# Kernel optimization log

Measured on AMD Instinct MI355X. Metric: run time of the kernel, lower is better.

The kernel has to match this reference:

```python
import jax, jax.numpy as jnp
import numpy as np

ANCHORS = np.array([[1.4940052559648322, 2.3598481287086823],
                    [4.0113013115312155, 5.760873975661669]], dtype=np.float32)
THRESH = 0.6
OBJ_SCALE = 5.0
NOOBJ_SCALE = 1.0


def setup_inputs() -> dict:
    key = jax.random.key(0)
    k1, k2, k3 = jax.random.split(key, 3)
    nB, nA, nH, nW = 128, 2, 128, 128
    output = jax.random.normal(k1, (nB, nA * 5, nH, nW), dtype=jnp.float32)
    xy = jax.random.uniform(k2, (nB, 2), jnp.float32, 0.1, 0.9)   # box centers, normalized
    wh = jax.random.uniform(k3, (nB, 2), jnp.float32, 0.05, 0.4)  # box sizes, normalized
    target = jnp.concatenate([xy, wh], axis=1)  # [nB, 4] = (x, y, w, h)
    anchors = jnp.asarray(ANCHORS)
    return {"output": output, "target": target, "anchors": anchors}


def reference(output, target, anchors):
    nB, _, nH, nW = output.shape
    nA = anchors.shape[0]
    # [nB, nA, nH, nW, 5]
    out = output.reshape(nB, nA, 5, nH, nW).transpose(0, 1, 3, 4, 2)
    x = jax.nn.sigmoid(out[..., 0])
    y = jax.nn.sigmoid(out[..., 1])
    w = out[..., 2]
    h = out[..., 3]
    conf = jax.nn.sigmoid(out[..., 4])

    # torch code uses .data / Variable() everywhere in target construction -> no grads flow there
    tgt = jax.lax.stop_gradient(target)
    anc = jax.lax.stop_gradient(anchors)
    sg = jax.lax.stop_gradient

    fW = jnp.asarray(nW, dtype=x.dtype)
    fH = jnp.asarray(nH, dtype=x.dtype)
    grid_x = jnp.arange(nW, dtype=x.dtype)[None, None, None, :]
    grid_y = jnp.arange(nH, dtype=x.dtype)[None, None, :, None]
    aw = anc[:, 0][None, :, None, None]
    ah = anc[:, 1][None, :, None, None]

    # detached predicted boxes in grid units (cx, cy, w, h)
    pb_x = sg(x) + grid_x
    pb_y = sg(y) + grid_y
    pb_w = jnp.exp(sg(w)) * aw
    pb_h = jnp.exp(sg(h)) * ah

    gt_x = tgt[:, 0] * fW
    gt_y = tgt[:, 1] * fH
    gt_w = tgt[:, 2] * fW
    gt_h = tgt[:, 3] * fH
    gx4 = gt_x[:, None, None, None]
    gy4 = gt_y[:, None, None, None]
    gw4 = gt_w[:, None, None, None]
    gh4 = gt_h[:, None, None, None]

    # vectorized bbox_iou (x1y1x2y2=False), faithful to the scalar torch loop
    mx = jnp.minimum(pb_x - pb_w * 0.5, gx4 - gw4 * 0.5)
    Mx = jnp.maximum(pb_x + pb_w * 0.5, gx4 + gw4 * 0.5)
    my = jnp.minimum(pb_y - pb_h * 0.5, gy4 - gh4 * 0.5)
    My = jnp.maximum(pb_y + pb_h * 0.5, gy4 + gh4 * 0.5)
    uw = Mx - mx
    uh = My - my
    cw = pb_w + gw4 - uw
    ch = pb_h + gh4 - uh
    carea = cw * ch
    uarea = pb_w * pb_h + gw4 * gh4 - carea
    iou = jnp.where((cw <= 0) | (ch <= 0), jnp.zeros((), x.dtype), carea / uarea)

    noobj_mask = iou <= THRESH  # [nB, nA, nH, nW]

    # best anchor per GT via wh-IoU (bbox_anchor_iou)
    inter = jnp.minimum(gt_w[:, None], anc[None, :, 0]) * jnp.minimum(gt_h[:, None], anc[None, :, 1])
    union = gt_w[:, None] * gt_h[:, None] + 1e-16 + anc[None, :, 0] * anc[None, :, 1] - inter
    best_n = jnp.argmax(inter / union, axis=1)  # [nB]

    gxi = gt_x.astype(jnp.int32)
    gyi = gt_y.astype(jnp.int32)
    b_idx = jnp.arange(nB)
    noobj_mask = noobj_mask.at[b_idx, best_n, gyi, gxi].set(False)

    tx = gt_x - jnp.floor(gt_x)
    ty = gt_y - jnp.floor(gt_y)
    tw = jnp.log(gt_w / anc[best_n, 0] + 1e-16)
    th = jnp.log(gt_h / anc[best_n, 1] + 1e-16)
    scale = 2.0 - tgt[:, 2] * tgt[:, 3]  # [nB]

    x_s = x[b_idx, best_n, gyi, gxi]
    y_s = y[b_idx, best_n, gyi, gxi]
    w_s = w[b_idx, best_n, gyi, gxi]
    h_s = h[b_idx, best_n, gyi, gxi]
    conf_s = conf[b_idx, best_n, gyi, gxi]

    loss_x = jnp.mean((x_s * scale - tx * scale) ** 2)
    loss_y = jnp.mean((y_s * scale - ty * scale) ** 2)
    loss_w = jnp.mean((w_s * scale - tw * scale) ** 2)
    loss_h = jnp.mean((h_s * scale - th * scale) ** 2)

    n_noobj = jnp.sum(noobj_mask).astype(conf.dtype)
    loss_conf = (OBJ_SCALE * jnp.mean((conf_s - 1.0) ** 2)
                 + NOOBJ_SCALE * jnp.sum(jnp.where(noobj_mask, conf * conf, 0.0)) / n_noobj)

    return loss_x + loss_y + loss_w + loss_h + loss_conf
```

## Files before the change

kernel.cpp:

```cpp
#include <hip/hip_runtime.h>

#define NB 128
#define NA 2
#define NH 128
#define NW 128
#define PLANE (NH * NW)
#define RTHRESH 0.6f
#define OBJ_SCALE 5.0f
#define NBLK 1024

__device__ __forceinline__ float sigm(float v) {
    return 1.0f / (1.0f + __expf(-v));
}

__device__ __forceinline__ void batch_const(const float* __restrict__ target,
                                            const float* __restrict__ anchors,
                                            int b,
                                            float& gx, float& gy, float& gw, float& gh,
                                            int& bn, int& gxi, int& gyi) {
    float t0 = target[b * 4 + 0], t1 = target[b * 4 + 1];
    float t2 = target[b * 4 + 2], t3 = target[b * 4 + 3];
    gx = t0 * (float)NW;
    gy = t1 * (float)NH;
    gw = t2 * (float)NW;
    gh = t3 * (float)NH;
    float a0w = anchors[0], a0h = anchors[1];
    float a1w = anchors[2], a1h = anchors[3];
    float i0 = fminf(gw, a0w) * fminf(gh, a0h);
    float u0 = gw * gh + 1e-16f + a0w * a0h - i0;
    float i1 = fminf(gw, a1w) * fminf(gh, a1h);
    float u1 = gw * gh + 1e-16f + a1w * a1h - i1;
    bn  = (i1 / u1 > i0 / u0) ? 1 : 0;
    gxi = (int)gx;
    gyi = (int)gy;
}

__global__ __launch_bounds__(256) void region_main(
        const float* __restrict__ out,
        const float* __restrict__ target,
        const float* __restrict__ anchors,
        float* __restrict__ psum,
        unsigned int* __restrict__ pcnt) {
    int bid = blockIdx.x, tid = threadIdx.x;
    int slab = bid >> 2, q = bid & 3;
    int b = slab >> 1, a = slab & 1;

    float gx, gy, gw, gh; int bn, gxi, gyi;
    batch_const(target, anchors, b, gx, gy, gw, gh, bn, gxi, gyi);
    float aw = anchors[a * 2 + 0];
    float ah = anchors[a * 2 + 1];

    const float* pb = out + (size_t)(b * 10 + a * 5) * PLANE + q * 4096 + tid * 4;

    float4 vx[4], vy[4], vw[4], vh[4], vc[4];
#pragma unroll
    for (int it = 0; it < 4; ++it) {
        const float* p = pb + it * 1024;
        vx[it] = *(const float4*)(p);
        vy[it] = *(const float4*)(p + 1 * PLANE);
        vw[it] = *(const float4*)(p + 2 * PLANE);
        vh[it] = *(const float4*)(p + 3 * PLANE);
        vc[it] = *(const float4*)(p + 4 * PLANE);
    }

    float gxm = gx - gw * 0.5f, gxM = gx + gw * 0.5f;
    float gym = gy - gh * 0.5f, gyM = gy + gh * 0.5f;
    float garea = gw * gh;
    bool a_sel = (a == bn);

    float lsum = 0.0f;
    int   lcnt = 0;

#pragma unroll
    for (int it = 0; it < 4; ++it) {
        const float* fx = (const float*)&vx[it];
        const float* fy = (const float*)&vy[it];
        const float* fw = (const float*)&vw[it];
        const float* fh = (const float*)&vh[it];
        const float* fc = (const float*)&vc[it];
        int pos0 = q * 4096 + it * 1024 + tid * 4;
#pragma unroll
        for (int e = 0; e < 4; ++e) {
            int pos = pos0 + e;
            int j = pos & 127, i = pos >> 7;
            float px = sigm(fx[e]) + (float)j;
            float py = sigm(fy[e]) + (float)i;
            float pw = __expf(fw[e]) * aw;
            float ph = __expf(fh[e]) * ah;
            float cf = sigm(fc[e]);

            float mx = fminf(px - pw * 0.5f, gxm);
            float Mx = fmaxf(px + pw * 0.5f, gxM);
            float my = fminf(py - ph * 0.5f, gym);
            float My = fmaxf(py + ph * 0.5f, gyM);
            float cw = pw + gw - (Mx - mx);
            float ch = ph + gh - (My - my);
            float iou = 0.0f;
            if (cw > 0.0f && ch > 0.0f) {
                float carea = cw * ch;
                iou = carea / (pw * ph + garea - carea);
            }
            bool noobj = (iou <= RTHRESH) && !(a_sel && i == gyi && j == gxi);
            if (noobj) { lsum += cf * cf; lcnt += 1; }
        }
    }

#pragma unroll
    for (int off = 32; off > 0; off >>= 1) {
        lsum += __shfl_down(lsum, off);
        lcnt += __shfl_down(lcnt, off);
    }
    __shared__ float ssum[4];
    __shared__ int   scnt[4];
    int wid = tid >> 6, lane = tid & 63;
    if (lane == 0) { ssum[wid] = lsum; scnt[wid] = lcnt; }
    __syncthreads();
    if (tid == 0) {
        psum[bid] = ssum[0] + ssum[1] + ssum[2] + ssum[3];
        pcnt[bid] = (unsigned int)(scnt[0] + scnt[1] + scnt[2] + scnt[3]);
    }
}

__global__ __launch_bounds__(1024) void region_final(
        const float* __restrict__ out,
        const float* __restrict__ target,
        const float* __restrict__ anchors,
        const float* __restrict__ psum,
        const unsigned int* __restrict__ pcnt,
        float* __restrict__ loss_out) {
    int t = threadIdx.x;
    float s = psum[t];
    unsigned int c = pcnt[t];

    float v = 0.0f;
    if (t < NB) {
        int b = t;
        float gx, gy, gw, gh; int bn, gxi, gyi;
        batch_const(target, anchors, b, gx, gy, gw, gh, bn, gxi, gyi);
        float tx = gx - floorf(gx);
        float ty = gy - floorf(gy);
        float aw = anchors[bn * 2 + 0];
        float ah = anchors[bn * 2 + 1];
        float tw = __logf(gw / aw + 1e-16f);
        float th = __logf(gh / ah + 1e-16f);
        float scale = 2.0f - target[b * 4 + 2] * target[b * 4 + 3];

        size_t base = (size_t)(b * 10 + bn * 5) * PLANE + (size_t)gyi * NW + (size_t)gxi;
        float xs = sigm(out[base]);
        float ys = sigm(out[base + 1 * PLANE]);
        float wr = out[base + 2 * PLANE];
        float hr = out[base + 3 * PLANE];
        float cs = sigm(out[base + 4 * PLANE]);

        float dx = (xs - tx) * scale;
        float dy = (ys - ty) * scale;
        float dw = (wr - tw) * scale;
        float dh = (hr - th) * scale;
        float dc = cs - 1.0f;
        v = dx * dx + dy * dy + dw * dw + dh * dh + OBJ_SCALE * dc * dc;
    }

#pragma unroll
    for (int off = 32; off > 0; off >>= 1) {
        s += __shfl_down(s, off);
        c += __shfl_down(c, off);
        v += __shfl_down(v, off);
    }
    __shared__ float ss[16];
    __shared__ unsigned int sc[16];
    __shared__ float sv[16];
    int wid = t >> 6, lane = t & 63;
    if (lane == 0) { ss[wid] = s; sc[wid] = c; sv[wid] = v; }
    __syncthreads();
    if (t < 16) {
        s = ss[t]; c = sc[t]; v = sv[t];
#pragma unroll
        for (int off = 8; off > 0; off >>= 1) {
            s += __shfl_down(s, off);
            c += __shfl_down(c, off);
            v += __shfl_down(v, off);
        }
        if (t == 0)
            loss_out[0] = v * (1.0f / (float)NB) + s / (float)c;
    }
}

extern "C" void kernel_launch(void* const* d_in, const int* in_sizes, int n_in,
                              void* d_out, int out_size, void* d_ws, size_t ws_size,
                              hipStream_t stream) {
    const float* output  = (const float*)d_in[0];
    const float* target  = (const float*)d_in[1];
    const float* anchors = (const float*)d_in[2];
    float* loss = (float*)d_out;

    float* psum = (float*)d_ws;
    unsigned int* pcnt = (unsigned int*)((char*)d_ws + NBLK * sizeof(float));

    region_main<<<NBLK, 256, 0, stream>>>(output, target, anchors, psum, pcnt);
    region_final<<<1, 1024, 0, stream>>>(output, target, anchors, psum, pcnt, loss);
}
```

Measured before the change: 124.9 us.

## Replace IoU division with multiply compare, use fast reciprocal sigmoid, prefetch per step

The IoU threshold test becomes a multiply-compare (carea <= 0.6*union) instead of a per-element division, and the sigmoid uses the hardware approximate reciprocal. The loads are rearranged into a one-step-ahead software prefetch in place of loading all 20 float4 values up front, which lowers register pressure. Row-index work is hoisted out of the inner element loop. The fast reciprocal and the reworked comparison can flip threshold decisions for borderline cells. The code also has a redundant 'part' expression that looks like leftover editing.

```diff
diff --git a/kernel.cpp b/kernel.cpp
--- a/kernel.cpp
+++ b/kernel.cpp
@@ -5,12 +5,11 @@
 #define NH 128
 #define NW 128
 #define PLANE (NH * NW)
-#define RTHRESH 0.6f
 #define OBJ_SCALE 5.0f
 #define NBLK 1024
 
 __device__ __forceinline__ float sigm(float v) {
-    return 1.0f / (1.0f + __expf(-v));
+    return __builtin_amdgcn_rcpf(1.0f + __expf(-v));
 }
 
 __device__ __forceinline__ void batch_const(const float* __restrict__ target,
@@ -41,8 +40,11 @@
         const float* __restrict__ anchors,
         float* __restrict__ psum,
         unsigned int* __restrict__ pcnt) {
-    int bid = blockIdx.x, tid = threadIdx.x;
-    int slab = bid >> 2, q = bid & 3;
+    int tid = threadIdx.x;
+    int bid = blockIdx.x;
+    int slab = bid >> 2;
+    int part = bid & 2 ? (bid & 3) : (bid & 3);
+    part = bid & 3;
     int b = slab >> 1, a = slab & 1;
 
     float gx, gy, gw, gh; int bn, gxi, gyi;
@@ -50,59 +52,71 @@
     float aw = anchors[a * 2 + 0];
     float ah = anchors[a * 2 + 1];
 
-    const float* pb = out + (size_t)(b * 10 + a * 5) * PLANE + q * 4096 + tid * 4;
-
-    float4 vx[4], vy[4], vw[4], vh[4], vc[4];
-#pragma unroll
-    for (int it = 0; it < 4; ++it) {
-        const float* p = pb + it * 1024;
-        vx[it] = *(const float4*)(p);
-        vy[it] = *(const float4*)(p + 1 * PLANE);
-        vw[it] = *(const float4*)(p + 2 * PLANE);
-        vh[it] = *(const float4*)(p + 3 * PLANE);
-        vc[it] = *(const float4*)(p + 4 * PLANE);
-    }
+    const float* pb = out + (size_t)(b * 10 + a * 5) * PLANE + part * 4096 + tid * 4;
+
+    float4 cx = *(const float4*)(pb);
+    float4 cy = *(const float4*)(pb + 1 * PLANE);
+    float4 cw4 = *(const float4*)(pb + 2 * PLANE);
+    float4 ch4 = *(const float4*)(pb + 3 * PLANE);
+    float4 cc = *(const float4*)(pb + 4 * PLANE);
 
     float gxm = gx - gw * 0.5f, gxM = gx + gw * 0.5f;
     float gym = gy - gh * 0.5f, gyM = gy + gh * 0.5f;
     float garea = gw * gh;
+    float uthresh_k = 0.6f;
     bool a_sel = (a == bn);
 
     float lsum = 0.0f;
     int   lcnt = 0;
 
 #pragma unroll
-    for (int it = 0; it < 4; ++it) {
-        const float* fx = (const float*)&vx[it];
-        const float* fy = (const float*)&vy[it];
-        const float* fw = (const float*)&vw[it];
-        const float* fh = (const float*)&vh[it];
-        const float* fc = (const float*)&vc[it];
-        int pos0 = q * 4096 + it * 1024 + tid * 4;
+    for (int s = 0; s < 4; ++s) {
+        float4 nx, ny, nw4, nh4, nc;
+        if (s < 3) {
+            const float* pn = pb + (s + 1) * 1024;
+            nx  = *(const float4*)(pn);
+            ny  = *(const float4*)(pn + 1 * PLANE);
+            nw4 = *(const float4*)(pn + 2 * PLANE);
+            nh4 = *(const float4*)(pn + 3 * PLANE);
+            nc  = *(const float4*)(pn + 4 * PLANE);
+        }
+
+        int pos0 = part * 4096 + s * 1024 + tid * 4;
+        int i  = pos0 >> 7;
+        int j0 = pos0 & 127;
+        float fi = (float)i;
+        bool row_sel = a_sel && (i == gyi);
+
+        const float* fx = (const float*)&cx;
+        const float* fy = (const float*)&cy;
+        const float* fw = (const float*)&cw4;
+        const float* fh = (const float*)&ch4;
+        const float* fc = (const float*)&cc;
+
 #pragma unroll
         for (int e = 0; e < 4; ++e) {
-            int pos = pos0 + e;
-            int j = pos & 127, i = pos >> 7;
-            float px = sigm(fx[e]) + (float)j;
-            float py = sigm(fy[e]) + (float)i;
+            float px = sigm(fx[e]) + (float)(j0 + e);
+            float py = sigm(fy[e]) + fi;
             float pw = __expf(fw[e]) * aw;
             float ph = __expf(fh[e]) * ah;
             float cf = sigm(fc[e]);
 
-            float mx = fminf(px - pw * 0.5f, gxm);
-            float Mx = fmaxf(px + pw * 0.5f, gxM);
-            float my = fminf(py - ph * 0.5f, gym);
-            float My = fmaxf(py + ph * 0.5f, gyM);
+            float pwh = pw * 0.5f, phh = ph * 0.5f;
+            float mx = fminf(px - pwh, gxm);
+            float Mx = fmaxf(px + pwh, gxM);
+            float my = fminf(py - phh, gym);
+            float My = fmaxf(py + phh, gyM);
             float cw = pw + gw - (Mx - mx);
             float ch = ph + gh - (My - my);
-            float iou = 0.0f;
-            if (cw > 0.0f && ch > 0.0f) {
-                float carea = cw * ch;
-                iou = carea / (pw * ph + garea - carea);
-            }
-            bool noobj = (iou <= RTHRESH) && !(a_sel && i == gyi && j == gxi);
+            float carea = cw * ch;
+            float uarea = pw * ph + garea - carea;
+            bool noobj = (cw <= 0.0f) || (ch <= 0.0f) ||
+                         (carea <= uthresh_k * uarea);
+            noobj = noobj && !(row_sel && (j0 + e) == gxi);
             if (noobj) { lsum += cf * cf; lcnt += 1; }
         }
+
+        if (s < 3) { cx = nx; cy = ny; cw4 = nw4; ch4 = nh4; cc = nc; }
     }
 
 #pragma unroll
```

Measured after the change: 121.8 us. 2.5% less time.
